# Performance work log

Hardware: AMD Instinct MI355X
Metric: run time of the kernel (lower is better)

Reference implementation:

```python
import jax, jax.numpy as jnp
import numpy as np

N_NODES = 50000
N_EDGES = 600000
N_REL = 8
D_IN = 128
D_OUT = 128


def setup_inputs() -> dict:
    key = jax.random.key(0)
    ks = jax.random.split(key, 12)
    s = 1.0 / np.sqrt(D_IN)
    s2 = 1.0 / np.sqrt(2 * D_IN)
    return {
        "x": jax.random.normal(ks[0], (N_NODES, D_IN), jnp.float32),
        "src": jax.random.randint(ks[1], (N_EDGES,), 0, N_NODES, jnp.int32),
        "dst": jax.random.randint(ks[2], (N_EDGES,), 0, N_NODES, jnp.int32),
        "etype": jax.random.randint(ks[3], (N_EDGES,), 0, N_REL, jnp.int32),
        "Wrel": jax.random.normal(ks[4], (N_REL, D_IN, D_OUT), jnp.float32) * s,
        "Wloop": jax.random.normal(ks[5], (D_IN, D_OUT), jnp.float32) * s,
        "brel": jax.random.normal(ks[6], (D_OUT,), jnp.float32) * s,
        "W1": jax.random.normal(ks[7], (2 * D_IN, 2 * D_IN), jnp.float32) * s2,
        "b1": jax.random.normal(ks[8], (2 * D_IN,), jnp.float32) * s2,
        "W2": jax.random.normal(ks[9], (2 * D_IN, D_OUT), jnp.float32) * s2,
        "b2": jax.random.normal(ks[10], (D_OUT,), jnp.float32) * s2,
    }


def rel_graph_conv(x, src, dst, etype, Wrel, Wloop, brel):
    # low_mem style: transform node features once per relation, then gather per edge.
    xW = jnp.einsum('ni,rio->rno', x, Wrel)          # [R, N, D_OUT]
    msg = xW[etype, src]                              # [E, D_OUT] gather by (rel, src)
    agg = jax.ops.segment_sum(msg, dst, num_segments=N_NODES)  # scatter-add to dst
    return agg + x @ Wloop + brel                     # self-loop + bias (DGL defaults)


def reference(x, src, dst, etype, Wrel, Wloop, brel, W1, b1, W2, b2):
    mid = rel_graph_conv(x, src, dst, etype, Wrel, Wloop, brel)
    h = jnp.concatenate([x, mid], axis=1)             # [N, 2*D_IN]
    h = jax.nn.relu(h @ W1 + b1)
    return h @ W2 + b2
```

## Files before the change

kernel.cpp:

```cpp
#include <hip/hip_runtime.h>

#define N_NODES 50000
#define N_EDGES 600000
#define N_REL 8
#define NT_PAD 50176
#define N_TILES 196

typedef __attribute__((ext_vector_type(8))) short bf16x8;
typedef __attribute__((ext_vector_type(4))) float f32x4;

__device__ __forceinline__ ushort f2b(float f) {
    union { float f; unsigned u; } v; v.f = f;
    unsigned r = v.u + 0x7FFFu + ((v.u >> 16) & 1u);
    return (ushort)(r >> 16);
}
__device__ __forceinline__ float b2f(ushort s) {
    union { unsigned u; float f; } v; v.u = ((unsigned)s) << 16;
    return v.f;
}
__device__ __forceinline__ float asf(unsigned u) {
    union { unsigned u; float f; } v; v.u = u;
    return v.f;
}


__global__ void conv_f32_bf16(const float* __restrict__ in, ushort* __restrict__ outb) {
    int i = (blockIdx.x * 256 + threadIdx.x) * 4;
    float4 f = *(const float4*)(in + i);
    ushort4 o; o.x = f2b(f.x); o.y = f2b(f.y); o.z = f2b(f.z); o.w = f2b(f.w);
    *(ushort4*)(outb + i) = o;
}

__global__ void transpose_wts3(const float* __restrict__ Wloop, const float* __restrict__ Wrel,
                               const float* __restrict__ W1, const float* __restrict__ W2,
                               ushort* __restrict__ wt) {
    int y = blockIdx.y;
    if (y == 0) {
        for (int idx = blockIdx.x * 256 + threadIdx.x; idx < 128 * 1152; idx += gridDim.x * 256) {
            int c = idx / 1152, kg = idx - c * 1152;
            float v = (kg < 1024) ? Wrel[(size_t)((kg >> 7) * 128 + (kg & 127)) * 128 + c]
                                  : Wloop[(size_t)(kg - 1024) * 128 + c];
            wt[idx] = f2b(v);
        }
    } else if (y == 1) {
        for (int idx = blockIdx.x * 256 + threadIdx.x; idx < 256 * 256; idx += gridDim.x * 256) {
            int c = idx >> 8, k = idx & 255;
            wt[147456 + idx] = f2b(W1[k * 256 + c]);
        }
    } else {
        for (int idx = blockIdx.x * 256 + threadIdx.x; idx < 128 * 256; idx += gridDim.x * 256) {
            int c = idx >> 8, k = idx & 255;
            wt[212992 + idx] = f2b(W2[k * 128 + c]);
        }
    }
}

template<int NPH, int KMODE, int AS, int CTOT, int OMODE>
__global__ __launch_bounds__(256, 4) void mfma_gemm(
        const ushort* __restrict__ A0, const ushort* __restrict__ A1,
        const ushort* __restrict__ Bt, const float* __restrict__ bias,
        void* __restrict__ outv) {
    __shared__ ushort bs[2][128 * 72];
    const int t = threadIdx.x;
    const int wave = t >> 6, lane = t & 63;
    const int lr = lane & 15, lg = lane >> 4;
    const int wr = (wave >> 1) * 32, wc = (wave & 1) * 64;
    const int row0 = blockIdx.x * 64;
    const int KTOT = NPH * 64;
    const ushort* Btb = Bt + (size_t)blockIdx.y * 128 * KTOT;
    const int sgk = (t & 7) * 8;
    const int sc0 = t >> 3;

#define STAGE_LOAD(p)                                                              \
    _Pragma("unroll")                                                              \
    for (int it = 0; it < 4; ++it)                                                 \
        sreg[it] = *(const bf16x8*)(Btb + (size_t)(sc0 + it * 32) * KTOT +         \
                                    (p) * 64 + sgk);

#define STAGE_WRITE(b)                                                             \
    _Pragma("unroll")                                                              \
    for (int it = 0; it < 4; ++it)                                                 \
        *(bf16x8*)(&bs[b][(sc0 + it * 32) * 72 + sgk]) = sreg[it];

#define LOAD_AF(p)                                                                 \
    {                                                                              \
        const ushort* Ap; int as_;                                                 \
        if (KMODE == 0) {                                                          \
            if ((p) < 16) { Ap = A0 + (p) * 64;        as_ = 1024; }               \
            else          { Ap = A1 + ((p) - 16) * 64; as_ = 128;  }               \
        } else if (KMODE == 1) {                                                   \
            if ((p) < NPH / 2) { Ap = A0 + (p) * 64;           as_ = AS; }         \
            else               { Ap = A1 + ((p) - NPH / 2) * 64; as_ = AS; }       \
        } else { Ap = A0 + (p) * 64; as_ = AS; }                                   \
        _Pragma("unroll")                                                          \
        for (int rt = 0; rt < 2; ++rt) {                                           \
            int ar = row0 + wr + rt * 16 + lr;                                     \
            if (ar >= N_NODES) ar = 0;                                             \
            _Pragma("unroll")                                                      \
            for (int kc = 0; kc < 2; ++kc)                                         \
                af[rt][kc] = *(const bf16x8*)(Ap + (size_t)ar * as_ + kc * 32 + lg * 8); \
        }                                                                          \
    }

    f32x4 acc[2][4];
#pragma unroll
    for (int rt = 0; rt < 2; ++rt)
#pragma unroll
        for (int nt = 0; nt < 4; ++nt) acc[rt][nt] = (f32x4){0.f, 0.f, 0.f, 0.f};

    bf16x8 af[2][2], sreg[4];

    STAGE_LOAD(0);
    STAGE_WRITE(0);
    __syncthreads();

#pragma unroll
    for (int p = 0; p < NPH; ++p) {
        if (p + 1 < NPH) STAGE_LOAD(p + 1);
        LOAD_AF(p);
        const ushort* bcur = bs[p & 1];
#pragma unroll
        for (int kc = 0; kc < 2; ++kc) {
            bf16x8 bf[4];
#pragma unroll
            for (int nt = 0; nt < 4; ++nt)
                bf[nt] = *(const bf16x8*)(bcur + (wc + nt * 16 + lr) * 72 + kc * 32 + lg * 8);
#pragma unroll
            for (int rt = 0; rt < 2; ++rt)
#pragma unroll
                for (int nt = 0; nt < 4; ++nt)
                    acc[rt][nt] = __builtin_amdgcn_mfma_f32_16x16x32_bf16(af[rt][kc], bf[nt], acc[rt][nt], 0, 0, 0);
        }
        if (p + 1 < NPH) STAGE_WRITE((p + 1) & 1);
        __syncthreads();
    }

    const int colbase = blockIdx.y * 128;
#pragma unroll
    for (int rt = 0; rt < 2; ++rt) {
#pragma unroll
        for (int nt = 0; nt < 4; ++nt) {
            const int col = colbase + wc + nt * 16 + lr;
            const float bv = bias[col];
#pragma unroll
            for (int j = 0; j < 4; ++j) {
                const int r = row0 + wr + rt * 16 + lg * 4 + j;
                if (r >= N_NODES) continue;
                float vv = acc[rt][nt][j] + bv;
                if (OMODE == 0) {
                    ((float*)outv)[(size_t)r * CTOT + col] = vv;
                } else if (OMODE == 2) {
                    ((ushort*)outv)[(size_t)r * CTOT + col] = f2b(fmaxf(vv, 0.f));
                } else {
                    ((ushort*)outv)[(size_t)r * 128 + col] = f2b(vv);
                }
            }
        }
    }
#undef STAGE_LOAD
#undef STAGE_WRITE
#undef LOAD_AF
}


__global__ void zero_cnt(int* __restrict__ cnt) {
    int i = blockIdx.x * 256 + threadIdx.x;
    if (i < NT_PAD) cnt[i] = 0;
}

__global__ void hist_dst(const int* __restrict__ dst, int* __restrict__ cnt) {
    int e = blockIdx.x * 256 + threadIdx.x;
    if (e < N_EDGES) atomicAdd(&cnt[dst[e]], 1);
}

__global__ void scan_tiles(const int* __restrict__ cnt, int* __restrict__ tincl, int* __restrict__ bsum) {
    __shared__ int s[256];
    int i = blockIdx.x * 256 + threadIdx.x;
    int v = cnt[i];
    s[threadIdx.x] = v;
    __syncthreads();
    for (int off = 1; off < 256; off <<= 1) {
        int add = (threadIdx.x >= off) ? s[threadIdx.x - off] : 0;
        __syncthreads();
        s[threadIdx.x] += add;
        __syncthreads();
    }
    tincl[i] = s[threadIdx.x];
    if (threadIdx.x == 255) bsum[blockIdx.x] = s[255];
}

__global__ void scan_bsum(const int* __restrict__ bsum, int* __restrict__ bex) {
    __shared__ int s[256];
    int v = (threadIdx.x < N_TILES) ? bsum[threadIdx.x] : 0;
    s[threadIdx.x] = v;
    __syncthreads();
    for (int off = 1; off < 256; off <<= 1) {
        int add = (threadIdx.x >= off) ? s[threadIdx.x - off] : 0;
        __syncthreads();
        s[threadIdx.x] += add;
        __syncthreads();
    }
    if (threadIdx.x < N_TILES) bex[threadIdx.x] = s[threadIdx.x] - v;
}

__global__ void finalize_base(const int* __restrict__ cnt, const int* __restrict__ tincl,
                              const int* __restrict__ bex, int* __restrict__ base,
                              int* __restrict__ cursor) {
    int i = blockIdx.x * 256 + threadIdx.x;
    int b = tincl[i] - cnt[i] + bex[blockIdx.x];
    base[i] = b; cursor[i] = b;
}

__global__ void scatter_ids(const int* __restrict__ src, const int* __restrict__ dst,
                            const int* __restrict__ et, int* __restrict__ cursor,
                            unsigned* __restrict__ sorted) {
    int e = blockIdx.x * 256 + threadIdx.x;
    if (e >= N_EDGES) return;
    int pos = atomicAdd(&cursor[dst[e]], 1);
    sorted[pos] = ((unsigned)src[e] << 3) | (unsigned)et[e];
}


#define ACC_ADD(sd, v)                                                       \
    {                                                                        \
        float lo = asf((v) << 16);                                           \
        float hi = asf((v) & 0xffff0000u);                                   \
        switch ((sd) & 7u) {                                                 \
            case 0: a0[0] += lo; a1[0] += hi; asm volatile(""); break;       \
            case 1: a0[1] += lo; a1[1] += hi; asm volatile(""); break;       \
            case 2: a0[2] += lo; a1[2] += hi; asm volatile(""); break;       \
            case 3: a0[3] += lo; a1[3] += hi; asm volatile(""); break;       \
            case 4: a0[4] += lo; a1[4] += hi; asm volatile(""); break;       \
            case 5: a0[5] += lo; a1[5] += hi; asm volatile(""); break;       \
            case 6: a0[6] += lo; a1[6] += hi; asm volatile(""); break;       \
            default: a0[7] += lo; a1[7] += hi; asm volatile(""); break;      \
        }                                                                    \
    }

__global__ __launch_bounds__(256) void gather_agg(
        const unsigned* __restrict__ sorted, const int* __restrict__ base,
        const int* __restrict__ cnt, const ushort* __restrict__ xbf,
        ushort* __restrict__ agg) {
    const int w = threadIdx.x >> 6, lane = threadIdx.x & 63;
    const int n = blockIdx.x * 4 + w;
    const int b = base[n], c = cnt[n];
    const int loff = lane * 2;

    float a0[8], a1[8];
#pragma unroll
    for (int r = 0; r < 8; ++r) { a0[r] = 0.f; a1[r] = 0.f; }

    const unsigned* sp = sorted + b;
    int i = 0;
    for (; i + 4 <= c; i += 4) {
        unsigned s0 = __builtin_amdgcn_readfirstlane(sp[i]);
        unsigned s1 = __builtin_amdgcn_readfirstlane(sp[i + 1]);
        unsigned s2 = __builtin_amdgcn_readfirstlane(sp[i + 2]);
        unsigned s3 = __builtin_amdgcn_readfirstlane(sp[i + 3]);
        unsigned v0 = *(const unsigned*)(xbf + ((size_t)(s0 >> 3) << 7) + loff);
        unsigned v1 = *(const unsigned*)(xbf + ((size_t)(s1 >> 3) << 7) + loff);
        unsigned v2 = *(const unsigned*)(xbf + ((size_t)(s2 >> 3) << 7) + loff);
        unsigned v3 = *(const unsigned*)(xbf + ((size_t)(s3 >> 3) << 7) + loff);
        ACC_ADD(s0, v0); ACC_ADD(s1, v1); ACC_ADD(s2, v2); ACC_ADD(s3, v3);
    }
    for (; i < c; ++i) {
        unsigned sd = __builtin_amdgcn_readfirstlane(sp[i]);
        unsigned v = *(const unsigned*)(xbf + ((size_t)(sd >> 3) << 7) + loff);
        ACC_ADD(sd, v);
    }
#pragma unroll
    for (int r = 0; r < 8; ++r) {
        unsigned pk = (unsigned)f2b(a0[r]) | ((unsigned)f2b(a1[r]) << 16);
        *(unsigned*)(agg + (size_t)n * 1024 + r * 128 + loff) = pk;
    }
}
#undef ACC_ADD


extern "C" void kernel_launch(void* const* d_in, const int* in_sizes, int n_in,
                              void* d_out, int out_size, void* d_ws, size_t ws_size,
                              hipStream_t stream) {
    const float* x     = (const float*)d_in[0];
    const int*   src   = (const int*)  d_in[1];
    const int*   dst   = (const int*)  d_in[2];
    const int*   etype = (const int*)  d_in[3];
    const float* Wrel  = (const float*)d_in[4];
    const float* Wloop = (const float*)d_in[5];
    const float* brel  = (const float*)d_in[6];
    const float* W1    = (const float*)d_in[7];
    const float* b1    = (const float*)d_in[8];
    const float* W2    = (const float*)d_in[9];
    const float* b2    = (const float*)d_in[10];
    float* out = (float*)d_out;

    char* ws = (char*)d_ws;
    ushort* agg   = (ushort*)ws;
    ushort* wt    = (ushort*)(ws + 102400000);
    char* meta    = ws + 102891520;
    int* cnt      = (int*)(meta);
    int* base     = (int*)(meta + 200704);
    int* cursor   = (int*)(meta + 401408);
    int* tincl    = (int*)(meta + 602112);
    int* bsum     = (int*)(meta + 802816);
    int* bex      = (int*)(meta + 803840);
    unsigned* sorted = (unsigned*)(meta + 804864);
    ushort* xbf   = (ushort*)(ws + 106096384);
    ushort* midbf = (ushort*)(ws + 118896384);

    const ushort* wst = wt;
    const ushort* w1t = wt + 147456;
    const ushort* w2t = wt + 212992;
    ushort* h = agg;

    conv_f32_bf16<<<6250, 256, 0, stream>>>(x, xbf);
    transpose_wts3<<<dim3(64, 3), 256, 0, stream>>>(Wloop, Wrel, W1, W2, wt);

    zero_cnt<<<N_TILES, 256, 0, stream>>>(cnt);
    hist_dst<<<(N_EDGES + 255) / 256, 256, 0, stream>>>(dst, cnt);
    scan_tiles<<<N_TILES, 256, 0, stream>>>(cnt, tincl, bsum);
    scan_bsum<<<1, 256, 0, stream>>>(bsum, bex);
    finalize_base<<<N_TILES, 256, 0, stream>>>(cnt, tincl, bex, base, cursor);
    scatter_ids<<<(N_EDGES + 255) / 256, 256, 0, stream>>>(src, dst, etype, cursor, sorted);

    gather_agg<<<N_NODES / 4, 256, 0, stream>>>(sorted, base, cnt, xbf, agg);

    mfma_gemm<18, 0, 0, 128, 4><<<dim3(782, 1), 256, 0, stream>>>(agg, xbf, wst, brel, (void*)midbf);

    mfma_gemm<4, 1, 128, 256, 2><<<dim3(782, 2), 256, 0, stream>>>(xbf, midbf, w1t, b1, (void*)h);

    mfma_gemm<4, 2, 256, 128, 0><<<dim3(782, 1), 256, 0, stream>>>(h, nullptr, w2t, b2, out);
}
```

Baseline: 214.5 us.

## Fold conv weights into W1 and fuse conv GEMM with first MLP layer

Precomputes combined weights (Wrel·W1b, Wloop·W1b + W1a) and a combined bias on the device, so the relational conv GEMM and the first MLP GEMM become a single 1152-deep GEMM producing 256 columns with ReLU. This removes the intermediate mid buffer write and read and one kernel launch. It also prefetches the next A fragments one phase ahead in the GEMM loop. In exchange the fused GEMM does more MFMA work per row (1152×256 instead of 1152×128 plus 256×256), and rounding the folded weights to bf16 changes numerics slightly.

```diff
diff --git a/kernel.cpp b/kernel.cpp
--- a/kernel.cpp
+++ b/kernel.cpp
@@ -31,27 +31,38 @@
     *(ushort4*)(outb + i) = o;
 }
 
-__global__ void transpose_wts3(const float* __restrict__ Wloop, const float* __restrict__ Wrel,
-                               const float* __restrict__ W1, const float* __restrict__ W2,
-                               ushort* __restrict__ wt) {
-    int y = blockIdx.y;
-    if (y == 0) {
-        for (int idx = blockIdx.x * 256 + threadIdx.x; idx < 128 * 1152; idx += gridDim.x * 256) {
-            int c = idx / 1152, kg = idx - c * 1152;
-            float v = (kg < 1024) ? Wrel[(size_t)((kg >> 7) * 128 + (kg & 127)) * 128 + c]
-                                  : Wloop[(size_t)(kg - 1024) * 128 + c];
-            wt[idx] = f2b(v);
-        }
-    } else if (y == 1) {
-        for (int idx = blockIdx.x * 256 + threadIdx.x; idx < 256 * 256; idx += gridDim.x * 256) {
-            int c = idx >> 8, k = idx & 255;
-            wt[147456 + idx] = f2b(W1[k * 256 + c]);
-        }
+__global__ void prep_w2t(const float* __restrict__ W2, ushort* __restrict__ w2t) {
+    int idx = blockIdx.x * 256 + threadIdx.x;
+    if (idx < 128 * 256) {
+        int c = idx >> 8, k = idx & 255;
+        w2t[(size_t)c * 256 + k] = f2b(W2[k * 128 + c]);
+    }
+}
+
+__global__ void wcomb_prep(const float* __restrict__ Wrel, const float* __restrict__ Wloop,
+                           const float* __restrict__ W1, const float* __restrict__ b1,
+                           const float* __restrict__ brel,
+                           ushort* __restrict__ wtf, float* __restrict__ bcomb) {
+    const int kg = blockIdx.x;
+    const int c = threadIdx.x;
+    if (kg < 1024) {
+        const float* wsrow = Wrel + (size_t)(kg >> 7) * 16384 + (size_t)(kg & 127) * 128;
+        float acc = 0.f;
+        for (int m = 0; m < 128; ++m)
+            acc += wsrow[m] * W1[(128 + m) * 256 + c];
+        wtf[(size_t)c * 1152 + 128 + kg] = f2b(acc);
+    } else if (kg < 1152) {
+        const int j = kg - 1024;
+        const float* wsrow = Wloop + (size_t)j * 128;
+        float acc = W1[j * 256 + c];
+        for (int m = 0; m < 128; ++m)
+            acc += wsrow[m] * W1[(128 + m) * 256 + c];
+        wtf[(size_t)c * 1152 + j] = f2b(acc);
     } else {
-        for (int idx = blockIdx.x * 256 + threadIdx.x; idx < 128 * 256; idx += gridDim.x * 256) {
-            int c = idx >> 8, k = idx & 255;
-            wt[212992 + idx] = f2b(W2[k * 128 + c]);
-        }
+        float acc = b1[c];
+        for (int m = 0; m < 128; ++m)
+            acc += brel[m] * W1[(128 + m) * 256 + c];
+        bcomb[c] = acc;
     }
 }
 
@@ -82,15 +93,12 @@
     for (int it = 0; it < 4; ++it)                                                 \
         *(bf16x8*)(&bs[b][(sc0 + it * 32) * 72 + sgk]) = sreg[it];
 
-#define LOAD_AF(p)                                                                 \
+#define LOAD_AF(p, dstf)                                                           \
     {                                                                              \
         const ushort* Ap; int as_;                                                 \
         if (KMODE == 0) {                                                          \
-            if ((p) < 16) { Ap = A0 + (p) * 64;        as_ = 1024; }               \
-            else          { Ap = A1 + ((p) - 16) * 64; as_ = 128;  }               \
-        } else if (KMODE == 1) {                                                   \
-            if ((p) < NPH / 2) { Ap = A0 + (p) * 64;           as_ = AS; }         \
-            else               { Ap = A1 + ((p) - NPH / 2) * 64; as_ = AS; }       \
+            if ((p) < 2) { Ap = A0 + (p) * 64;       as_ = 128;  }                 \
+            else         { Ap = A1 + ((p) - 2) * 64; as_ = 1024; }                 \
         } else { Ap = A0 + (p) * 64; as_ = AS; }                                   \
         _Pragma("unroll")                                                          \
         for (int rt = 0; rt < 2; ++rt) {                                           \
@@ -98,7 +106,7 @@
             if (ar >= N_NODES) ar = 0;                                             \
             _Pragma("unroll")                                                      \
             for (int kc = 0; kc < 2; ++kc)                                         \
-                af[rt][kc] = *(const bf16x8*)(Ap + (size_t)ar * as_ + kc * 32 + lg * 8); \
+                dstf[rt][kc] = *(const bf16x8*)(Ap + (size_t)ar * as_ + kc * 32 + lg * 8); \
         }                                                                          \
     }
 
@@ -108,16 +116,19 @@
 #pragma unroll
         for (int nt = 0; nt < 4; ++nt) acc[rt][nt] = (f32x4){0.f, 0.f, 0.f, 0.f};
 
-    bf16x8 af[2][2], sreg[4];
+    bf16x8 af[2][2], afn[2][2], sreg[4];
 
     STAGE_LOAD(0);
+    LOAD_AF(0, af);
     STAGE_WRITE(0);
     __syncthreads();
 
 #pragma unroll
     for (int p = 0; p < NPH; ++p) {
-        if (p + 1 < NPH) STAGE_LOAD(p + 1);
-        LOAD_AF(p);
+        if (p + 1 < NPH) {
+            STAGE_LOAD(p + 1);
+            LOAD_AF(p + 1, afn);
+        }
         const ushort* bcur = bs[p & 1];
 #pragma unroll
         for (int kc = 0; kc < 2; ++kc) {
@@ -133,6 +144,12 @@
         }
         if (p + 1 < NPH) STAGE_WRITE((p + 1) & 1);
         __syncthreads();
+        if (p + 1 < NPH) {
+#pragma unroll
+            for (int rt = 0; rt < 2; ++rt)
+#pragma unroll
+                for (int kc = 0; kc < 2; ++kc) af[rt][kc] = afn[rt][kc];
+        }
     }
 
     const int colbase = blockIdx.y * 128;
@@ -149,10 +166,8 @@
                 float vv = acc[rt][nt][j] + bv;
                 if (OMODE == 0) {
                     ((float*)outv)[(size_t)r * CTOT + col] = vv;
-                } else if (OMODE == 2) {
+                } else {
                     ((ushort*)outv)[(size_t)r * CTOT + col] = f2b(fmaxf(vv, 0.f));
-                } else {
-                    ((ushort*)outv)[(size_t)r * 128 + col] = f2b(vv);
                 }
             }
         }
@@ -295,8 +310,10 @@
 
     char* ws = (char*)d_ws;
     ushort* agg   = (ushort*)ws;
-    ushort* wt    = (ushort*)(ws + 102400000);
-    char* meta    = ws + 102891520;
+    ushort* wtf   = (ushort*)(ws + 102400000);
+    ushort* w2t   = (ushort*)(ws + 102989824);
+    float*  bcomb = (float*) (ws + 103055360);
+    char* meta    = ws + 103056384;
     int* cnt      = (int*)(meta);
     int* base     = (int*)(meta + 200704);
     int* cursor   = (int*)(meta + 401408);
@@ -304,16 +321,12 @@
     int* bsum     = (int*)(meta + 802816);
     int* bex      = (int*)(meta + 803840);
     unsigned* sorted = (unsigned*)(meta + 804864);
-    ushort* xbf   = (ushort*)(ws + 106096384);
-    ushort* midbf = (ushort*)(ws + 118896384);
-
-    const ushort* wst = wt;
-    const ushort* w1t = wt + 147456;
-    const ushort* w2t = wt + 212992;
-    ushort* h = agg;
+    ushort* xbf   = (ushort*)(ws + 106261248);
+    ushort* h     = (ushort*)(ws + 119061248);
 
     conv_f32_bf16<<<6250, 256, 0, stream>>>(x, xbf);
-    transpose_wts3<<<dim3(64, 3), 256, 0, stream>>>(Wloop, Wrel, W1, W2, wt);
+    prep_w2t<<<128, 256, 0, stream>>>(W2, w2t);
+    wcomb_prep<<<1153, 256, 0, stream>>>(Wrel, Wloop, W1, b1, brel, wtf, bcomb);
 
     zero_cnt<<<N_TILES, 256, 0, stream>>>(cnt);
     hist_dst<<<(N_EDGES + 255) / 256, 256, 0, stream>>>(dst, cnt);
@@ -324,9 +337,7 @@
 
     gather_agg<<<N_NODES / 4, 256, 0, stream>>>(sorted, base, cnt, xbf, agg);
 
-    mfma_gemm<18, 0, 0, 128, 4><<<dim3(782, 1), 256, 0, stream>>>(agg, xbf, wst, brel, (void*)midbf);
-
-    mfma_gemm<4, 1, 128, 256, 2><<<dim3(782, 2), 256, 0, stream>>>(xbf, midbf, w1t, b1, (void*)h);
+    mfma_gemm<18, 0, 0, 256, 2><<<dim3(782, 2), 256, 0, stream>>>(xbf, agg, wtf, bcomb, (void*)h);
 
     mfma_gemm<4, 2, 256, 128, 0><<<dim3(782, 1), 256, 0, stream>>>(h, nullptr, w2t, b2, out);
 }
```

After: 235.1 us. +9.6%, slower.

## Fuse the two MLP GEMMs into one kernel and prefetch A fragments

Applied to the files above, without the earlier changes.

Replaces the two separate MLP GEMM launches with a single kernel. It computes relu(h@W1+b1) for a 64-row tile, keeps the hidden activations in LDS, then multiplies by W2 in place, so the bf16 hidden tensor never goes through global memory. The generic GEMM also now loads A fragments for the next phase one step early, so register loads overlap the MFMAs. The costs are more registers and LDS per block, and 2-blocks-per-CU launch bounds that may reduce occupancy.

```diff
diff --git a/kernel.cpp b/kernel.cpp
--- a/kernel.cpp
+++ b/kernel.cpp
@@ -82,15 +82,12 @@
     for (int it = 0; it < 4; ++it)                                                 \
         *(bf16x8*)(&bs[b][(sc0 + it * 32) * 72 + sgk]) = sreg[it];
 
-#define LOAD_AF(p)                                                                 \
+#define LOAD_AF(p, dstf)                                                           \
     {                                                                              \
         const ushort* Ap; int as_;                                                 \
         if (KMODE == 0) {                                                          \
             if ((p) < 16) { Ap = A0 + (p) * 64;        as_ = 1024; }               \
             else          { Ap = A1 + ((p) - 16) * 64; as_ = 128;  }               \
-        } else if (KMODE == 1) {                                                   \
-            if ((p) < NPH / 2) { Ap = A0 + (p) * 64;           as_ = AS; }         \
-            else               { Ap = A1 + ((p) - NPH / 2) * 64; as_ = AS; }       \
         } else { Ap = A0 + (p) * 64; as_ = AS; }                                   \
         _Pragma("unroll")                                                          \
         for (int rt = 0; rt < 2; ++rt) {                                           \
@@ -98,7 +95,7 @@
             if (ar >= N_NODES) ar = 0;                                             \
             _Pragma("unroll")                                                      \
             for (int kc = 0; kc < 2; ++kc)                                         \
-                af[rt][kc] = *(const bf16x8*)(Ap + (size_t)ar * as_ + kc * 32 + lg * 8); \
+                dstf[rt][kc] = *(const bf16x8*)(Ap + (size_t)ar * as_ + kc * 32 + lg * 8); \
         }                                                                          \
     }
 
@@ -108,16 +105,19 @@
 #pragma unroll
         for (int nt = 0; nt < 4; ++nt) acc[rt][nt] = (f32x4){0.f, 0.f, 0.f, 0.f};
 
-    bf16x8 af[2][2], sreg[4];
+    bf16x8 af[2][2], afn[2][2], sreg[4];
 
     STAGE_LOAD(0);
+    LOAD_AF(0, af);
     STAGE_WRITE(0);
     __syncthreads();
 
 #pragma unroll
     for (int p = 0; p < NPH; ++p) {
-        if (p + 1 < NPH) STAGE_LOAD(p + 1);
-        LOAD_AF(p);
+        if (p + 1 < NPH) {
+            STAGE_LOAD(p + 1);
+            LOAD_AF(p + 1, afn);
+        }
         const ushort* bcur = bs[p & 1];
 #pragma unroll
         for (int kc = 0; kc < 2; ++kc) {
@@ -133,6 +133,12 @@
         }
         if (p + 1 < NPH) STAGE_WRITE((p + 1) & 1);
         __syncthreads();
+        if (p + 1 < NPH) {
+#pragma unroll
+            for (int rt = 0; rt < 2; ++rt)
+#pragma unroll
+                for (int kc = 0; kc < 2; ++kc) af[rt][kc] = afn[rt][kc];
+        }
     }
 
     const int colbase = blockIdx.y * 128;
@@ -149,8 +155,6 @@
                 float vv = acc[rt][nt][j] + bv;
                 if (OMODE == 0) {
                     ((float*)outv)[(size_t)r * CTOT + col] = vv;
-                } else if (OMODE == 2) {
-                    ((ushort*)outv)[(size_t)r * CTOT + col] = f2b(fmaxf(vv, 0.f));
                 } else {
                     ((ushort*)outv)[(size_t)r * 128 + col] = f2b(vv);
                 }
@@ -160,6 +164,163 @@
 #undef STAGE_LOAD
 #undef STAGE_WRITE
 #undef LOAD_AF
+}
+
+__global__ __launch_bounds__(256, 2) void mlp_fused(
+        const ushort* __restrict__ xbf, const ushort* __restrict__ midbf,
+        const ushort* __restrict__ w1t, const ushort* __restrict__ w2t,
+        const float* __restrict__ b1, const float* __restrict__ b2,
+        float* __restrict__ out) {
+    __shared__ ushort ldsA[256 * 72];
+    __shared__ ushort ldsB[256 * 72];
+    const int t = threadIdx.x;
+    const int wave = t >> 6, lane = t & 63;
+    const int lr = lane & 15, lg = lane >> 4;
+    const int row0 = blockIdx.x * 64;
+    const int sgk = (t & 7) * 8;
+    const int sc0 = t >> 3;
+
+    {
+        const int wr = (wave >> 1) * 32, wc = (wave & 1) * 128;
+        f32x4 acc[2][8];
+#pragma unroll
+        for (int rt = 0; rt < 2; ++rt)
+#pragma unroll
+            for (int nt = 0; nt < 8; ++nt) acc[rt][nt] = (f32x4){0.f, 0.f, 0.f, 0.f};
+        bf16x8 af[2][2], afn[2][2], sreg[8];
+
+#define S1_LOAD(p)                                                                 \
+    _Pragma("unroll")                                                              \
+    for (int it = 0; it < 8; ++it)                                                 \
+        sreg[it] = *(const bf16x8*)(w1t + (size_t)(sc0 + it * 32) * 256 + (p) * 64 + sgk);
+
+#define S1_WRITE(bptr)                                                             \
+    _Pragma("unroll")                                                              \
+    for (int it = 0; it < 8; ++it)                                                 \
+        *(bf16x8*)((bptr) + (sc0 + it * 32) * 72 + sgk) = sreg[it];
+
+#define S1_AF(p, dstf)                                                             \
+    {                                                                              \
+        const ushort* Ap = ((p) < 2) ? (xbf + (p) * 64) : (midbf + ((p) - 2) * 64);\
+        _Pragma("unroll")                                                          \
+        for (int rt = 0; rt < 2; ++rt) {                                           \
+            int ar = row0 + wr + rt * 16 + lr;                                     \
+            if (ar >= N_NODES) ar = 0;                                             \
+            _Pragma("unroll")                                                      \
+            for (int kc = 0; kc < 2; ++kc)                                         \
+                dstf[rt][kc] = *(const bf16x8*)(Ap + (size_t)ar * 128 + kc * 32 + lg * 8); \
+        }                                                                          \
+    }
+
+        S1_LOAD(0); S1_AF(0, af); S1_WRITE(ldsA);
+        __syncthreads();
+#pragma unroll
+        for (int p = 0; p < 4; ++p) {
+            if (p < 3) { S1_LOAD(p + 1); S1_AF(p + 1, afn); }
+            const ushort* bc = (p & 1) ? ldsB : ldsA;
+#pragma unroll
+            for (int kc = 0; kc < 2; ++kc) {
+                bf16x8 bf[8];
+#pragma unroll
+                for (int nt = 0; nt < 8; ++nt)
+                    bf[nt] = *(const bf16x8*)(bc + (wc + nt * 16 + lr) * 72 + kc * 32 + lg * 8);
+#pragma unroll
+                for (int rt = 0; rt < 2; ++rt)
+#pragma unroll
+                    for (int nt = 0; nt < 8; ++nt)
+                        acc[rt][nt] = __builtin_amdgcn_mfma_f32_16x16x32_bf16(af[rt][kc], bf[nt], acc[rt][nt], 0, 0, 0);
+            }
+            if (p < 3) { S1_WRITE(((p + 1) & 1) ? ldsB : ldsA); }
+            __syncthreads();
+            if (p < 3) {
+#pragma unroll
+                for (int rt = 0; rt < 2; ++rt)
+#pragma unroll
+                    for (int kc = 0; kc < 2; ++kc) af[rt][kc] = afn[rt][kc];
+            }
+        }
+#pragma unroll
+        for (int rt = 0; rt < 2; ++rt)
+#pragma unroll
+            for (int nt = 0; nt < 8; ++nt) {
+                const int col = wc + nt * 16 + lr;
+                const float bv = b1[col];
+#pragma unroll
+                for (int j = 0; j < 4; ++j) {
+                    const int hr = wr + rt * 16 + lg * 4 + j;
+                    ldsA[hr * 264 + col] = f2b(fmaxf(acc[rt][nt][j] + bv, 0.f));
+                }
+            }
+#undef S1_LOAD
+#undef S1_WRITE
+#undef S1_AF
+    }
+
+    {
+        bf16x8 sreg2[4];
+#define S2_LOAD(p)                                                                 \
+    _Pragma("unroll")                                                              \
+    for (int it = 0; it < 4; ++it)                                                 \
+        sreg2[it] = *(const bf16x8*)(w2t + (size_t)(sc0 + it * 32) * 256 + (p) * 64 + sgk);
+
+#define S2_WRITE(half)                                                             \
+    _Pragma("unroll")                                                              \
+    for (int it = 0; it < 4; ++it)                                                 \
+        *(bf16x8*)(ldsB + (half) * (128 * 72) + (sc0 + it * 32) * 72 + sgk) = sreg2[it];
+
+        S2_LOAD(0); S2_WRITE(0);
+        __syncthreads();
+
+        const int wr = (wave >> 1) * 32, wc = (wave & 1) * 64;
+        f32x4 acc[2][4];
+#pragma unroll
+        for (int rt = 0; rt < 2; ++rt)
+#pragma unroll
+            for (int nt = 0; nt < 4; ++nt) acc[rt][nt] = (f32x4){0.f, 0.f, 0.f, 0.f};
+        bf16x8 af[2][2];
+
+#pragma unroll
+        for (int p = 0; p < 4; ++p) {
+            if (p < 3) S2_LOAD(p + 1);
+#pragma unroll
+            for (int rt = 0; rt < 2; ++rt) {
+                const int ar = wr + rt * 16 + lr;
+#pragma unroll
+                for (int kc = 0; kc < 2; ++kc)
+                    af[rt][kc] = *(const bf16x8*)(ldsA + ar * 264 + p * 64 + kc * 32 + lg * 8);
+            }
+            const ushort* bc = ldsB + (p & 1) * (128 * 72);
+#pragma unroll
+            for (int kc = 0; kc < 2; ++kc) {
+                bf16x8 bf[4];
+#pragma unroll
+                for (int nt = 0; nt < 4; ++nt)
+                    bf[nt] = *(const bf16x8*)(bc + (wc + nt * 16 + lr) * 72 + kc * 32 + lg * 8);
+#pragma unroll
+                for (int rt = 0; rt < 2; ++rt)
+#pragma unroll
+                    for (int nt = 0; nt < 4; ++nt)
+                        acc[rt][nt] = __builtin_amdgcn_mfma_f32_16x16x32_bf16(af[rt][kc], bf[nt], acc[rt][nt], 0, 0, 0);
+            }
+            if (p < 3) S2_WRITE((p + 1) & 1);
+            __syncthreads();
+        }
+#pragma unroll
+        for (int rt = 0; rt < 2; ++rt)
+#pragma unroll
+            for (int nt = 0; nt < 4; ++nt) {
+                const int col = wc + nt * 16 + lr;
+                const float bv = b2[col];
+#pragma unroll
+                for (int j = 0; j < 4; ++j) {
+                    const int r = row0 + wr + rt * 16 + lg * 4 + j;
+                    if (r < N_NODES)
+                        out[(size_t)r * 128 + col] = acc[rt][nt][j] + bv;
+                }
+            }
+#undef S2_LOAD
+#undef S2_WRITE
+    }
 }
 
 
@@ -310,7 +471,6 @@
     const ushort* wst = wt;
     const ushort* w1t = wt + 147456;
     const ushort* w2t = wt + 212992;
-    ushort* h = agg;
 
     conv_f32_bf16<<<6250, 256, 0, stream>>>(x, xbf);
     transpose_wts3<<<dim3(64, 3), 256, 0, stream>>>(Wloop, Wrel, W1, W2, wt);
@@ -326,7 +486,5 @@
 
     mfma_gemm<18, 0, 0, 128, 4><<<dim3(782, 1), 256, 0, stream>>>(agg, xbf, wst, brel, (void*)midbf);
 
-    mfma_gemm<4, 1, 128, 256, 2><<<dim3(782, 2), 256, 0, stream>>>(xbf, midbf, w1t, b1, (void*)h);
-
-    mfma_gemm<4, 2, 256, 128, 0><<<dim3(782, 1), 256, 0, stream>>>(h, nullptr, w2t, b2, out);
-}
+    mlp_fused<<<782, 256, 0, stream>>>(xbf, midbf, w1t, w2t, b1, b2, out);
+}
```

After: 207.4 us. 1.03x faster.
